# Kernel optimization log

Measured on AMD Instinct MI355X. Metric: run time of the kernel, lower is better.

Reference implementation:

```python
import jax, jax.numpy as jnp
import numpy as np

N = 8192
F_IN = 256
F_OUT = 64
ALPHA = 0.2  # LeakyReLU negative slope
NEG_INF = -9e15


def setup_inputs() -> dict:
    key = jax.random.key(0)
    k1, k2, k3, k4 = jax.random.split(key, 4)
    h = jax.random.normal(k1, (N, F_IN), dtype=jnp.float32)
    adj = jax.random.randint(k2, (N, N), 0, 2, dtype=jnp.int32)
    W = jax.random.normal(k3, (F_IN, F_OUT), dtype=jnp.float32) * 0.1
    a = jax.random.normal(k4, (2 * F_OUT, 1), dtype=jnp.float32) * 0.1
    return {"h": h, "adj": adj, "W": W, "a": a}


def reference(h, adj, W, a):
    # Wh: [N, F_out]
    Wh = h @ W
    # e_ij = LeakyReLU(a1 . Wh_i + a2 . Wh_j); same math as the O(N^2*2F)
    # concat in the original, computed via two [N] gathers + broadcast add.
    f_src = Wh @ a[:F_OUT, 0]   # [N] contribution of node i (row)
    f_dst = Wh @ a[F_OUT:, 0]   # [N] contribution of node j (col)
    e = f_src[:, None] + f_dst[None, :]          # [N, N]
    e = jnp.where(e > 0, e, ALPHA * e)           # LeakyReLU
    # masked softmax over neighbors (dim=1)
    e = jnp.where(adj > 0, e, NEG_INF)
    attention = jax.nn.softmax(e, axis=1)        # [N, N]
    h_prime = attention @ Wh                     # [N, F_out]
    # concat=True -> ELU
    return jax.nn.elu(h_prime)
```

## Files before the change

### kernel.cpp

```cpp
#include <hip/hip_runtime.h>
#include <math.h>

#define N 8192
#define FIN 256
#define FOUT 64
#define ALPHA 0.2f
#define LOG2E 1.442695040888963f

typedef float f32x4 __attribute__((ext_vector_type(4)));
typedef _Float16 f16x8 __attribute__((ext_vector_type(8)));

union F16V { uint4 u; int4 i; f16x8 h; };

__device__ __forceinline__ unsigned pack_f16(float a, float b) {
    union { _Float16 h; unsigned short u; } ca, cb;
    ca.h = (_Float16)a; cb.h = (_Float16)b;
    return (unsigned)ca.u | ((unsigned)cb.u << 16);
}
__device__ __forceinline__ float wcalc(int av, float fsr, float g) {
    float e = fsr + g;
    float le = e > 0.f ? e : ALPHA * e;
    float r = __builtin_exp2f(fmaf(le, LOG2E, -4.0f));
    return av != 0 ? r : 0.f;
}

__global__ __launch_bounds__(512) void gat_prep(
    const float* __restrict__ h, const float* __restrict__ W,
    const float* __restrict__ a,
    float* __restrict__ fsrc, float* __restrict__ fdst,
    uint4* __restrict__ Bp)
{
    __shared__ float sWh[32][FOUT + 1];
    const int t = threadIdx.x;
    const int f = t & 63;
    const int wq = t >> 6;
    const int row0 = blockIdx.x * 32;
    const int rbase = row0 + wq * 4;

    float acc[4] = {0.f, 0.f, 0.f, 0.f};
    for (int k0 = 0; k0 < FIN; k0 += 4) {
        const float w0 = W[(k0 + 0) * FOUT + f];
        const float w1 = W[(k0 + 1) * FOUT + f];
        const float w2 = W[(k0 + 2) * FOUT + f];
        const float w3 = W[(k0 + 3) * FOUT + f];
#pragma unroll
        for (int rr = 0; rr < 4; ++rr) {
            const float4 hv = *reinterpret_cast<const float4*>(
                &h[(size_t)(rbase + rr) * FIN + k0]);
            acc[rr] = fmaf(hv.x, w0, acc[rr]);
            acc[rr] = fmaf(hv.y, w1, acc[rr]);
            acc[rr] = fmaf(hv.z, w2, acc[rr]);
            acc[rr] = fmaf(hv.w, w3, acc[rr]);
        }
    }
    const float as = a[f], ad = a[FOUT + f];
#pragma unroll
    for (int rr = 0; rr < 4; ++rr) {
        sWh[wq * 4 + rr][f] = acc[rr];
        float fs = acc[rr] * as, fd = acc[rr] * ad;
#pragma unroll
        for (int off = 1; off < 64; off <<= 1) {
            fs += __shfl_xor(fs, off, 64);
            fd += __shfl_xor(fd, off, 64);
        }
        if (f == 0) { fsrc[rbase + rr] = fs; fdst[rbase + rr] = fd; }
    }
    __syncthreads();
    if (t < 256) {
        const int ft = t >> 6;
        const int l = t & 63;
        const int li = l & 15, g = l >> 4;
        float v[8];
#pragma unroll
        for (int e = 0; e < 8; ++e) v[e] = sWh[g * 8 + e][ft * 16 + li];
        uint4 pk;
        pk.x = pack_f16(v[0], v[1]);
        pk.y = pack_f16(v[2], v[3]);
        pk.z = pack_f16(v[4], v[5]);
        pk.w = pack_f16(v[6], v[7]);
        Bp[(size_t)(blockIdx.x * 4 + ft) * 64 + l] = pk;
    }
}

struct Regs { int4 a0, a1; float4 g0, g1; uint4 b0, b1, b2, b3; };

__global__ __launch_bounds__(512, 4) void gat_main(
    const int* __restrict__ adj,
    const uint4* __restrict__ Bp,
    const float* __restrict__ fsrc, const float* __restrict__ fdst,
    float* __restrict__ out)
{
    __shared__ float accbuf[8][4][64][4];
    __shared__ float zbuf[8][16];
    __shared__ float Zfin[16];

    const int t = threadIdx.x;
    const int l = t & 63;
    const int w = t >> 6;
    const int row0 = blockIdx.x * 16;
    const int r = l & 15;
    const int kg8 = (l >> 4) << 3;
    const int jwbase = w * 1024;
    const int cgbase = w * 32;
    const float fsr = fsrc[row0 + r];
    const size_t adjrow = (size_t)(row0 + r) * N;

    f32x4 acc0 = {0.f, 0.f, 0.f, 0.f};
    f32x4 acc1 = {0.f, 0.f, 0.f, 0.f};
    f32x4 acc2 = {0.f, 0.f, 0.f, 0.f};
    f32x4 acc3 = {0.f, 0.f, 0.f, 0.f};
    float zacc = 0.f;
    Regs RA, RB;

#define LOADG(cl, S)                                                           \
    {                                                                          \
        const int j0_ = jwbase + (cl) * 32;                                    \
        S.a0 = *reinterpret_cast<const int4*>(&adj[adjrow + j0_ + kg8]);       \
        S.a1 = *reinterpret_cast<const int4*>(&adj[adjrow + j0_ + kg8 + 4]);   \
        S.g0 = *reinterpret_cast<const float4*>(&fdst[j0_ + kg8]);             \
        S.g1 = *reinterpret_cast<const float4*>(&fdst[j0_ + kg8 + 4]);         \
        const uint4* bp_ = Bp + ((size_t)(cgbase + (cl)) * 4) * 64 + l;        \
        S.b0 = bp_[0];                                                         \
        S.b1 = bp_[64];                                                        \
        S.b2 = bp_[128];                                                       \
        S.b3 = bp_[192];                                                       \
    }

#define COMPUTE(S)                                                             \
    {                                                                          \
        const float w0 = wcalc(S.a0.x, fsr, S.g0.x);                           \
        const float w1 = wcalc(S.a0.y, fsr, S.g0.y);                           \
        const float w2 = wcalc(S.a0.z, fsr, S.g0.z);                           \
        const float w3 = wcalc(S.a0.w, fsr, S.g0.w);                           \
        const float w4 = wcalc(S.a1.x, fsr, S.g1.x);                           \
        const float w5 = wcalc(S.a1.y, fsr, S.g1.y);                           \
        const float w6 = wcalc(S.a1.z, fsr, S.g1.z);                           \
        const float w7 = wcalc(S.a1.w, fsr, S.g1.w);                           \
        zacc += (w0 + w1) + (w2 + w3) + ((w4 + w5) + (w6 + w7));               \
        F16V av, b0v, b1v, b2v, b3v;                                           \
        av.u.x = pack_f16(w0, w1); av.u.y = pack_f16(w2, w3);                  \
        av.u.z = pack_f16(w4, w5); av.u.w = pack_f16(w6, w7);                  \
        b0v.u = S.b0; b1v.u = S.b1; b2v.u = S.b2; b3v.u = S.b3;                \
        __builtin_amdgcn_s_setprio(1);                                         \
        acc0 = __builtin_amdgcn_mfma_f32_16x16x32_f16(av.h, b0v.h, acc0, 0, 0, 0); \
        acc1 = __builtin_amdgcn_mfma_f32_16x16x32_f16(av.h, b1v.h, acc1, 0, 0, 0); \
        acc2 = __builtin_amdgcn_mfma_f32_16x16x32_f16(av.h, b2v.h, acc2, 0, 0, 0); \
        acc3 = __builtin_amdgcn_mfma_f32_16x16x32_f16(av.h, b3v.h, acc3, 0, 0, 0); \
        __builtin_amdgcn_s_setprio(0);                                         \
    }

    LOADG(0, RA);
    LOADG(1, RB);
    for (int c = 0; c < 32; c += 2) {
        COMPUTE(RA);
        if (c + 2 < 32) LOADG(c + 2, RA);
        COMPUTE(RB);
        if (c + 3 < 32) LOADG(c + 3, RB);
    }
#undef LOADG
#undef COMPUTE

    zacc += __shfl_xor(zacc, 16, 64);
    zacc += __shfl_xor(zacc, 32, 64);
    if (l < 16) zbuf[w][l] = zacc;
    *reinterpret_cast<f32x4*>(&accbuf[w][0][l][0]) = acc0;
    *reinterpret_cast<f32x4*>(&accbuf[w][1][l][0]) = acc1;
    *reinterpret_cast<f32x4*>(&accbuf[w][2][l][0]) = acc2;
    *reinterpret_cast<f32x4*>(&accbuf[w][3][l][0]) = acc3;
    __syncthreads();
    if (t < 16) {
        float z = 0.f;
#pragma unroll
        for (int w2 = 0; w2 < 8; ++w2) z += zbuf[w2][t];
        Zfin[t] = z;
    }
    __syncthreads();

#pragma unroll
    for (int e0 = 0; e0 < 2; ++e0) {
        const int e = t + e0 * 512;
        const int rr = e >> 6, f2 = e & 63;
        const int c = f2 >> 4;
        const int ln = (f2 & 15) | ((rr >> 2) << 4);
        const int rg = rr & 3;
        float s = 0.f;
#pragma unroll
        for (int w2 = 0; w2 < 8; ++w2) s += accbuf[w2][c][ln][rg];
        const float hp = s / Zfin[rr];
        out[(size_t)(row0 + rr) * FOUT + f2] = hp > 0.f ? hp : expm1f(hp);
    }
}

extern "C" void kernel_launch(void* const* d_in, const int* in_sizes, int n_in,
                              void* d_out, int out_size, void* d_ws, size_t ws_size,
                              hipStream_t stream) {
    const float* h   = (const float*)d_in[0];
    const int*   adj = (const int*)d_in[1];
    const float* W   = (const float*)d_in[2];
    const float* a   = (const float*)d_in[3];
    float* out = (float*)d_out;

    float* ws = (float*)d_ws;
    float* fsrc = ws;
    float* fdst = fsrc + N;
    uint4* Bp = (uint4*)(fdst + N);

    gat_prep<<<dim3(N / 32), dim3(512), 0, stream>>>(h, W, a, fsrc, fdst, Bp);
    gat_main<<<dim3(N / 16), dim3(512), 0, stream>>>(adj, Bp, fsrc, fdst, out);
}
```

Measured before the change: 103.1 us.

## Precompute adjacency as packed bitmask in separate kernel before attention pass

Adds a pre-pass kernel that reads the int32 adjacency matrix and packs each group of 8 entries into one byte. The main attention kernel then loads one byte per 8 neighbours instead of two int4 vectors, shrinking its global traffic and register footprint. The full adjacency matrix is still read once per call by the new kernel, so total memory traffic does not drop. It adds a kernel launch, a mask write and a serialisation point, in exchange for a lighter main loop.

New measurement: 111.7 us. +8.4%, slower.

```diff
diff --git a/kernel.cpp b/kernel.cpp
--- a/kernel.cpp
+++ b/kernel.cpp
@@ -10,7 +10,7 @@
 typedef float f32x4 __attribute__((ext_vector_type(4)));
 typedef _Float16 f16x8 __attribute__((ext_vector_type(8)));
 
-union F16V { uint4 u; int4 i; f16x8 h; };
+union F16V { uint4 u; f16x8 h; };
 
 __device__ __forceinline__ unsigned pack_f16(float a, float b) {
     union { _Float16 h; unsigned short u; } ca, cb;
@@ -22,6 +22,24 @@
     float le = e > 0.f ? e : ALPHA * e;
     float r = __builtin_exp2f(fmaf(le, LOG2E, -4.0f));
     return av != 0 ? r : 0.f;
+}
+
+__global__ __launch_bounds__(256) void gat_mask(
+    const int* __restrict__ adj, unsigned char* __restrict__ mask8)
+{
+    const size_t tid = (size_t)blockIdx.x * 256 + threadIdx.x;
+    const int4 v0 = *reinterpret_cast<const int4*>(&adj[tid * 8]);
+    const int4 v1 = *reinterpret_cast<const int4*>(&adj[tid * 8 + 4]);
+    unsigned m = 0;
+    m |= (v0.x != 0) ? 1u : 0u;
+    m |= (v0.y != 0) ? 2u : 0u;
+    m |= (v0.z != 0) ? 4u : 0u;
+    m |= (v0.w != 0) ? 8u : 0u;
+    m |= (v1.x != 0) ? 16u : 0u;
+    m |= (v1.y != 0) ? 32u : 0u;
+    m |= (v1.z != 0) ? 64u : 0u;
+    m |= (v1.w != 0) ? 128u : 0u;
+    mask8[tid] = (unsigned char)m;
 }
 
 __global__ __launch_bounds__(512) void gat_prep(
@@ -82,10 +100,10 @@
     }
 }
 
-struct Regs { int4 a0, a1; float4 g0, g1; uint4 b0, b1, b2, b3; };
+struct Regs { unsigned m8; float4 g0, g1; uint4 b0, b1, b2, b3; };
 
 __global__ __launch_bounds__(512, 4) void gat_main(
-    const int* __restrict__ adj,
+    const unsigned char* __restrict__ mask8,
     const uint4* __restrict__ Bp,
     const float* __restrict__ fsrc, const float* __restrict__ fdst,
     float* __restrict__ out)
@@ -99,11 +117,12 @@
     const int w = t >> 6;
     const int row0 = blockIdx.x * 16;
     const int r = l & 15;
-    const int kg8 = (l >> 4) << 3;
+    const int g16 = l >> 4;
+    const int kg8 = g16 << 3;
     const int jwbase = w * 1024;
     const int cgbase = w * 32;
     const float fsr = fsrc[row0 + r];
-    const size_t adjrow = (size_t)(row0 + r) * N;
+    const size_t mrow = (size_t)(row0 + r) * 1024 + (jwbase >> 3) + g16;
 
     f32x4 acc0 = {0.f, 0.f, 0.f, 0.f};
     f32x4 acc1 = {0.f, 0.f, 0.f, 0.f};
@@ -115,11 +134,10 @@
 #define LOADG(cl, S)                                                           \
     {                                                                          \
         const int j0_ = jwbase + (cl) * 32;                                    \
-        S.a0 = *reinterpret_cast<const int4*>(&adj[adjrow + j0_ + kg8]);       \
-        S.a1 = *reinterpret_cast<const int4*>(&adj[adjrow + j0_ + kg8 + 4]);   \
+        S.m8 = mask8[mrow + (cl) * 4];                                         \
         S.g0 = *reinterpret_cast<const float4*>(&fdst[j0_ + kg8]);             \
         S.g1 = *reinterpret_cast<const float4*>(&fdst[j0_ + kg8 + 4]);         \
-        const uint4* bp_ = Bp + ((size_t)(cgbase + (cl)) * 4) * 64 + l;        \
+        const uint4* bp_ = Bp + (size_t)(cgbase + (cl)) * 4 * 64 + l;          \
         S.b0 = bp_[0];                                                         \
         S.b1 = bp_[64];                                                        \
         S.b2 = bp_[128];                                                       \
@@ -128,14 +146,14 @@
 
 #define COMPUTE(S)                                                             \
     {                                                                          \
-        const float w0 = wcalc(S.a0.x, fsr, S.g0.x);                           \
-        const float w1 = wcalc(S.a0.y, fsr, S.g0.y);                           \
-        const float w2 = wcalc(S.a0.z, fsr, S.g0.z);                           \
-        const float w3 = wcalc(S.a0.w, fsr, S.g0.w);                           \
-        const float w4 = wcalc(S.a1.x, fsr, S.g1.x);                           \
-        const float w5 = wcalc(S.a1.y, fsr, S.g1.y);                           \
-        const float w6 = wcalc(S.a1.z, fsr, S.g1.z);                           \
-        const float w7 = wcalc(S.a1.w, fsr, S.g1.w);                           \
+        const float w0 = wcalc((int)(S.m8 & 1u),   fsr, S.g0.x);               \
+        const float w1 = wcalc((int)(S.m8 & 2u),   fsr, S.g0.y);               \
+        const float w2 = wcalc((int)(S.m8 & 4u),   fsr, S.g0.z);               \
+        const float w3 = wcalc((int)(S.m8 & 8u),   fsr, S.g0.w);               \
+        const float w4 = wcalc((int)(S.m8 & 16u),  fsr, S.g1.x);               \
+        const float w5 = wcalc((int)(S.m8 & 32u),  fsr, S.g1.y);               \
+        const float w6 = wcalc((int)(S.m8 & 64u),  fsr, S.g1.z);               \
+        const float w7 = wcalc((int)(S.m8 & 128u), fsr, S.g1.w);               \
         zacc += (w0 + w1) + (w2 + w3) + ((w4 + w5) + (w6 + w7));               \
         F16V av, b0v, b1v, b2v, b3v;                                           \
         av.u.x = pack_f16(w0, w1); av.u.y = pack_f16(w2, w3);                  \
@@ -204,7 +222,9 @@
     float* fsrc = ws;
     float* fdst = fsrc + N;
     uint4* Bp = (uint4*)(fdst + N);
-
+    unsigned char* mask8 = (unsigned char*)(Bp + 65536);
+
+    gat_mask<<<dim3((N / 8) * (N / 256)), dim3(256), 0, stream>>>(adj, mask8);
     gat_prep<<<dim3(N / 32), dim3(512), 0, stream>>>(h, W, a, fsrc, fdst, Bp);
-    gat_main<<<dim3(N / 16), dim3(512), 0, stream>>>(adj, Bp, fsrc, fdst, out);
-}
+    gat_main<<<dim3(N / 16), dim3(512), 0, stream>>>(mask8, Bp, fsrc, fdst, out);
+}
```

## Stage adjacency as bitmask in LDS with coalesced prologue loads

Applied to the files above, without the earlier changes.

Before the main loop, all threads cooperatively read the block's 16 adjacency rows with fully coalesced int4 loads and pack them into 32-bit bitmasks in shared memory. Each wave then reads its mask words once and extracts per-chunk bits, so the pipelined loop only loads fdst and Bp. The column chunks are also permuted so the prologue loads are contiguous, and the shared buffer is reused for the final reduction. The whole adjacency stream now sits in a serialized prologue ahead of compute, which reduces overlap of the dominant memory traffic with MFMA work.

Measured after the change: 103.5 us. Within noise of the previous version (+0.4%).

```diff
diff --git a/kernel.cpp b/kernel.cpp
--- a/kernel.cpp
+++ b/kernel.cpp
@@ -7,21 +7,25 @@
 #define ALPHA 0.2f
 #define LOG2E 1.442695040888963f
 
+#define FMPITCH 65
+#define FMWORDS (64 * FMPITCH)
+#define SMEM_BYTES 33280
+
 typedef float f32x4 __attribute__((ext_vector_type(4)));
 typedef _Float16 f16x8 __attribute__((ext_vector_type(8)));
 
-union F16V { uint4 u; int4 i; f16x8 h; };
+union F16V { uint4 u; f16x8 h; };
 
 __device__ __forceinline__ unsigned pack_f16(float a, float b) {
     union { _Float16 h; unsigned short u; } ca, cb;
     ca.h = (_Float16)a; cb.h = (_Float16)b;
     return (unsigned)ca.u | ((unsigned)cb.u << 16);
 }
-__device__ __forceinline__ float wcalc(int av, float fsr, float g) {
+__device__ __forceinline__ float wcalc(unsigned av, float fsr, float g) {
     float e = fsr + g;
     float le = e > 0.f ? e : ALPHA * e;
     float r = __builtin_exp2f(fmaf(le, LOG2E, -4.0f));
-    return av != 0 ? r : 0.f;
+    return av != 0u ? r : 0.f;
 }
 
 __global__ __launch_bounds__(512) void gat_prep(
@@ -82,7 +86,7 @@
     }
 }
 
-struct Regs { int4 a0, a1; float4 g0, g1; uint4 b0, b1, b2, b3; };
+struct Regs { float4 g0, g1; uint4 b0, b1, b2, b3; };
 
 __global__ __launch_bounds__(512, 4) void gat_main(
     const int* __restrict__ adj,
@@ -90,20 +94,49 @@
     const float* __restrict__ fsrc, const float* __restrict__ fdst,
     float* __restrict__ out)
 {
-    __shared__ float accbuf[8][4][64][4];
-    __shared__ float zbuf[8][16];
-    __shared__ float Zfin[16];
+    __shared__ __align__(16) char smem[SMEM_BYTES];
 
     const int t = threadIdx.x;
     const int l = t & 63;
     const int w = t >> 6;
     const int row0 = blockIdx.x * 16;
+    unsigned* fm = reinterpret_cast<unsigned*>(smem);
+
+    {
+        const int srow = t >> 5;
+        const int c5 = t & 31;
+        const int c0 = c5 >> 2;
+        const int slot = c5 & 3;
+        const int lcons = slot * 16 + srow;
+        const size_t adjrow = (size_t)(row0 + srow) * N;
+#pragma unroll
+        for (int w8 = 0; w8 < 8; ++w8) {
+            unsigned a32 = 0;
+#pragma unroll
+            for (int q = 0; q < 4; ++q) {
+                const size_t o = adjrow + (w8 * 4 + q) * 256 + c5 * 8;
+                const int4 v0 = *reinterpret_cast<const int4*>(&adj[o]);
+                const int4 v1 = *reinterpret_cast<const int4*>(&adj[o + 4]);
+                unsigned m = 0;
+                m |= (v0.x != 0) ? 1u : 0u;
+                m |= (v0.y != 0) ? 2u : 0u;
+                m |= (v0.z != 0) ? 4u : 0u;
+                m |= (v0.w != 0) ? 8u : 0u;
+                m |= (v1.x != 0) ? 16u : 0u;
+                m |= (v1.y != 0) ? 32u : 0u;
+                m |= (v1.z != 0) ? 64u : 0u;
+                m |= (v1.w != 0) ? 128u : 0u;
+                a32 |= m << (8 * q);
+            }
+            fm[(w8 * 8 + c0) * FMPITCH + lcons] = a32;
+        }
+    }
+
     const int r = l & 15;
     const int kg8 = (l >> 4) << 3;
     const int jwbase = w * 1024;
     const int cgbase = w * 32;
     const float fsr = fsrc[row0 + r];
-    const size_t adjrow = (size_t)(row0 + r) * N;
 
     f32x4 acc0 = {0.f, 0.f, 0.f, 0.f};
     f32x4 acc1 = {0.f, 0.f, 0.f, 0.f};
@@ -112,30 +145,32 @@
     float zacc = 0.f;
     Regs RA, RB;
 
-#define LOADG(cl, S)                                                           \
+#define CL(c) (((c) & 3) * 8 + ((c) >> 2))
+
+#define LOADG(c, S)                                                            \
     {                                                                          \
-        const int j0_ = jwbase + (cl) * 32;                                    \
-        S.a0 = *reinterpret_cast<const int4*>(&adj[adjrow + j0_ + kg8]);       \
-        S.a1 = *reinterpret_cast<const int4*>(&adj[adjrow + j0_ + kg8 + 4]);   \
+        const int cl_ = CL(c);                                                 \
+        const int j0_ = jwbase + cl_ * 32;                                     \
         S.g0 = *reinterpret_cast<const float4*>(&fdst[j0_ + kg8]);             \
         S.g1 = *reinterpret_cast<const float4*>(&fdst[j0_ + kg8 + 4]);         \
-        const uint4* bp_ = Bp + ((size_t)(cgbase + (cl)) * 4) * 64 + l;        \
+        const uint4* bp_ = Bp + (size_t)(cgbase + cl_) * 4 * 64 + l;           \
         S.b0 = bp_[0];                                                         \
         S.b1 = bp_[64];                                                        \
         S.b2 = bp_[128];                                                       \
         S.b3 = bp_[192];                                                       \
     }
 
-#define COMPUTE(S)                                                             \
+#define COMPUTE(c, S)                                                          \
     {                                                                          \
-        const float w0 = wcalc(S.a0.x, fsr, S.g0.x);                           \
-        const float w1 = wcalc(S.a0.y, fsr, S.g0.y);                           \
-        const float w2 = wcalc(S.a0.z, fsr, S.g0.z);                           \
-        const float w3 = wcalc(S.a0.w, fsr, S.g0.w);                           \
-        const float w4 = wcalc(S.a1.x, fsr, S.g1.x);                           \
-        const float w5 = wcalc(S.a1.y, fsr, S.g1.y);                           \
-        const float w6 = wcalc(S.a1.z, fsr, S.g1.z);                           \
-        const float w7 = wcalc(S.a1.w, fsr, S.g1.w);                           \
+        const unsigned m8 = (fmw[(c) >> 2] >> (8 * ((c) & 3))) & 0xffu;        \
+        const float w0 = wcalc(m8 & 1u,   fsr, S.g0.x);                        \
+        const float w1 = wcalc(m8 & 2u,   fsr, S.g0.y);                        \
+        const float w2 = wcalc(m8 & 4u,   fsr, S.g0.z);                        \
+        const float w3 = wcalc(m8 & 8u,   fsr, S.g0.w);                        \
+        const float w4 = wcalc(m8 & 16u,  fsr, S.g1.x);                        \
+        const float w5 = wcalc(m8 & 32u,  fsr, S.g1.y);                        \
+        const float w6 = wcalc(m8 & 64u,  fsr, S.g1.z);                        \
+        const float w7 = wcalc(m8 & 128u, fsr, S.g1.w);                        \
         zacc += (w0 + w1) + (w2 + w3) + ((w4 + w5) + (w6 + w7));               \
         F16V av, b0v, b1v, b2v, b3v;                                           \
         av.u.x = pack_f16(w0, w1); av.u.y = pack_f16(w2, w3);                  \
@@ -151,27 +186,41 @@
 
     LOADG(0, RA);
     LOADG(1, RB);
+    asm volatile("s_waitcnt lgkmcnt(0)" ::: "memory");
+    __builtin_amdgcn_s_barrier();
+
+    unsigned fmw[8];
+#pragma unroll
+    for (int g = 0; g < 8; ++g) fmw[g] = fm[(w * 8 + g) * FMPITCH + l];
+
+#pragma unroll
     for (int c = 0; c < 32; c += 2) {
-        COMPUTE(RA);
+        COMPUTE(c, RA);
         if (c + 2 < 32) LOADG(c + 2, RA);
-        COMPUTE(RB);
+        COMPUTE(c + 1, RB);
         if (c + 3 < 32) LOADG(c + 3, RB);
     }
 #undef LOADG
 #undef COMPUTE
+#undef CL
+
+    float* accbuf = reinterpret_cast<float*>(smem);
+    float* zbuf = reinterpret_cast<float*>(smem + 32768);
+    __shared__ float Zfin[16];
 
     zacc += __shfl_xor(zacc, 16, 64);
     zacc += __shfl_xor(zacc, 32, 64);
-    if (l < 16) zbuf[w][l] = zacc;
-    *reinterpret_cast<f32x4*>(&accbuf[w][0][l][0]) = acc0;
-    *reinterpret_cast<f32x4*>(&accbuf[w][1][l][0]) = acc1;
-    *reinterpret_cast<f32x4*>(&accbuf[w][2][l][0]) = acc2;
-    *reinterpret_cast<f32x4*>(&accbuf[w][3][l][0]) = acc3;
+    __syncthreads();
+    if (l < 16) zbuf[w * 16 + l] = zacc;
+    *reinterpret_cast<f32x4*>(&accbuf[((w * 4 + 0) * 64 + l) * 4]) = acc0;
+    *reinterpret_cast<f32x4*>(&accbuf[((w * 4 + 1) * 64 + l) * 4]) = acc1;
+    *reinterpret_cast<f32x4*>(&accbuf[((w * 4 + 2) * 64 + l) * 4]) = acc2;
+    *reinterpret_cast<f32x4*>(&accbuf[((w * 4 + 3) * 64 + l) * 4]) = acc3;
     __syncthreads();
     if (t < 16) {
         float z = 0.f;
 #pragma unroll
-        for (int w2 = 0; w2 < 8; ++w2) z += zbuf[w2][t];
+        for (int w2 = 0; w2 < 8; ++w2) z += zbuf[w2 * 16 + t];
         Zfin[t] = z;
     }
     __syncthreads();
@@ -185,7 +234,8 @@
         const int rg = rr & 3;
         float s = 0.f;
 #pragma unroll
-        for (int w2 = 0; w2 < 8; ++w2) s += accbuf[w2][c][ln][rg];
+        for (int w2 = 0; w2 < 8; ++w2)
+            s += accbuf[((w2 * 4 + c) * 64 + ln) * 4 + rg];
         const float hp = s / Zfin[rr];
         out[(size_t)(row0 + rr) * FOUT + f2] = hp > 0.f ? hp : expm1f(hp);
     }
```
